# Optimization experiments

Measured on AMD Instinct MI355X. Metric: run time of the kernel, lower is better.

The kernel has to match this reference:

```python
import jax, jax.numpy as jnp
import numpy as np


def setup_inputs() -> dict:
    key = jax.random.key(0)
    k1, k2, k3 = jax.random.split(key, 3)
    B, C, H, W = 256, 1, 512, 512
    SIZE, OUT = 512, 1
    x = jax.random.normal(k1, (B, C, H, W), dtype=jnp.float32)
    weights = jax.random.normal(k2, (SIZE, 4 * C, OUT), dtype=jnp.float32)
    biases = jax.random.normal(k3, (SIZE, OUT), dtype=jnp.float32)
    return {"x": x, "weights": weights, "biases": biases}


def _corner_ring_means(x, size):
    """Mean of the L-shaped ring between the (i)x(i) and (i-1)x(i-1) corner
    squares, for all four corners, computed via a summed-area table.
    Returns [B, size, 4*C] with corner order (tl, tr, bl, br), matching the
    original torch cat along the channel axis."""
    B, C = x.shape[0], x.shape[1]
    idx = jnp.arange(size)

    def corner_square_sums(y):
        # summed-area table anchored at top-left of y
        S = jnp.cumsum(jnp.cumsum(y, axis=2), axis=3)
        # S[..., i-1, i-1] = sum of y[:, :, :i, :i]
        return S[:, :, idx, idx]  # [B, C, size]

    tl = corner_square_sums(x)
    tr = corner_square_sums(x[:, :, :, ::-1])
    bl = corner_square_sums(x[:, :, ::-1, :])
    br = corner_square_sums(x[:, :, ::-1, ::-1])
    sq = jnp.stack([tl, tr, bl, br], axis=-1)  # [B, C, size, 4]

    # ring sum_i = square_sum_i - square_sum_{i-1}
    prev = jnp.concatenate([jnp.zeros_like(sq[:, :, :1]), sq[:, :, :-1]], axis=2)
    # ring pixel count: i*i - (i-1)*(i-1) = 2i - 1
    denom = (2 * jnp.arange(1, size + 1) - 1).astype(x.dtype)
    means = (sq - prev) / denom[None, None, :, None]  # [B, C, size, 4]

    # match torch cat(dim=2) of four [B, size, C] tensors -> [B, size, 4*C]
    return jnp.transpose(means, (0, 2, 3, 1)).reshape(B, size, 4 * C)


def reference(x, weights, biases):
    size = weights.shape[0]
    feats = _corner_ring_means(x, size)               # [B, size, 4]
    # F.linear(x_i, weights[i].T, biases[i]) == x_i @ weights[i] + biases[i]
    out = jnp.einsum('bsf,sfo->bso', feats, weights) + biases[None]
    out = jax.nn.relu(out)                            # per-index activation
    # torch cat(dim=1) of [B, out] chunks then squeeze(-1); out=1 -> [B, size]
    return out.reshape(x.shape[0], -1)
```

## Files before the change

### kernel.cpp

```cpp
#include <hip/hip_runtime.h>


#define HH 512
#define WW 512
#define NRING 512
#define NB (4 * NRING)

template<bool PARTIALS>
__global__ __launch_bounds__(256)
void ring_sum_kernel(const float* __restrict__ x, float* __restrict__ ws) {
    __shared__ float bins[NB];
    __shared__ float sc[4][64][17];
    const int tid  = threadIdx.x;
    const int lane = tid & 63;
    const int wave = tid >> 6;
    const int b     = blockIdx.x >> 3;
    const int chunk = blockIdx.x & 7;

    for (int t = tid; t < NB; t += 256) bins[t] = 0.f;
    __syncthreads();

    float vTL[8] = {0,0,0,0,0,0,0,0};
    float vTR[8] = {0,0,0,0,0,0,0,0};
    float vBL[8] = {0,0,0,0,0,0,0,0};
    float vBR[8] = {0,0,0,0,0,0,0,0};
    float rTL[16], rTR[16], rBL[16], rBR[16];
    #pragma unroll
    for (int k = 0; k < 16; ++k) { rTL[k]=0.f; rTR[k]=0.f; rBL[k]=0.f; rBR[k]=0.f; }

    const float4* img = (const float4*)x + (size_t)b * (HH * WW / 4);
    const int cA = 4 * lane;
    const int cB = 256 + 4 * lane;
    const int rbase = chunk * 64 + wave * 16;
    const bool top = (rbase < 256);

    float4 bufA[3], bufB[3];
    {
        const float4* rp0 = img + (size_t)rbase * (WW / 4);
        bufA[0] = rp0[lane];  bufB[0] = rp0[64 + lane];
        const float4* rp1 = img + (size_t)(rbase + 1) * (WW / 4);
        bufA[1] = rp1[lane];  bufB[1] = rp1[64 + lane];
    }

    #pragma unroll
    for (int k = 0; k < 16; ++k) {
        const int cur = k % 3, nx = (k + 2) % 3;
        if (k < 14) {
            const float4* rp = img + (size_t)(rbase + k + 2) * (WW / 4);
            bufA[nx] = rp[lane];  bufB[nx] = rp[64 + lane];
        }
        const int r = rbase + k;
        const int s = 511 - r;
        const float4 a  = bufA[cur];
        const float4 bb = bufB[cur];

        if (top) {
            #pragma unroll
            for (int e = 0; e < 4; ++e) {
                float v = (&a.x)[e]; int c = cA + e;
                rBL[k] += v;
                vTR[e] += v;
                float sel  = (c <= r) ? v : 0.f; rTL[k] += sel;  vTL[e] += v - sel;
                float sel2 = (c >= r) ? v : 0.f; rBR[k] += sel2; vBR[e] += v - sel2;
            }
            #pragma unroll
            for (int e = 0; e < 4; ++e) {
                float v = (&bb.x)[e]; int c = cB + e;
                rBR[k] += v;
                vTL[4 + e] += v;
                float sel  = (c >= s) ? v : 0.f; rTR[k] += sel;  vTR[4 + e] += v - sel;
                float sel2 = (c <= s) ? v : 0.f; rBL[k] += sel2; vBL[4 + e] += v - sel2;
            }
        } else {
            #pragma unroll
            for (int e = 0; e < 4; ++e) {
                float v = (&a.x)[e]; int c = cA + e;
                rTL[k] += v;
                vBR[e] += v;
                float sel  = (c >= s) ? v : 0.f; rTR[k] += sel;  vTR[e] += v - sel;
                float sel2 = (c <= s) ? v : 0.f; rBL[k] += sel2; vBL[e] += v - sel2;
            }
            #pragma unroll
            for (int e = 0; e < 4; ++e) {
                float v = (&bb.x)[e]; int c = cB + e;
                rTR[k] += v;
                vBL[4 + e] += v;
                float sel  = (c <= r) ? v : 0.f; rTL[k] += sel;  vTL[4 + e] += v - sel;
                float sel2 = (c >= r) ? v : 0.f; rBR[k] += sel2; vBR[4 + e] += v - sel2;
            }
        }
    }

    const int q  = lane >> 4;
    const int kk = lane & 15;
#define REDUCE_CORNER(ARR, CIDX, RING_OF_KK)                                   \
    {                                                                          \
        _Pragma("unroll")                                                      \
        for (int j = 0; j < 16; ++j) sc[wave][lane][j] = ARR[j];               \
        __syncthreads();                                                       \
        float acc = 0.f;                                                       \
        _Pragma("unroll")                                                      \
        for (int l = 0; l < 16; ++l) acc += sc[wave][q * 16 + l][kk];          \
        acc += __shfl_down(acc, 32);                                           \
        acc += __shfl_down(acc, 16);                                           \
        if (lane < 16) atomicAdd(&bins[(CIDX) * NRING + (RING_OF_KK)], acc);   \
        __syncthreads();                                                       \
    }
    REDUCE_CORNER(rTL, 0, rbase + kk)
    REDUCE_CORNER(rTR, 1, rbase + kk)
    REDUCE_CORNER(rBL, 2, 511 - (rbase + kk))
    REDUCE_CORNER(rBR, 3, 511 - (rbase + kk))
#undef REDUCE_CORNER

    #pragma unroll
    for (int e = 0; e < 8; ++e) {
        int c = (e < 4) ? (cA + e) : (cB + e - 4);
        atomicAdd(&bins[0 * NRING + c],         vTL[e]);
        atomicAdd(&bins[1 * NRING + (511 - c)], vTR[e]);
        atomicAdd(&bins[2 * NRING + c],         vBL[e]);
        atomicAdd(&bins[3 * NRING + (511 - c)], vBR[e]);
    }
    __syncthreads();

    if (PARTIALS) {
        float* outp = ws + ((size_t)b * 8 + chunk) * NB;
        for (int t = tid; t < NB; t += 256) outp[t] = bins[t];
    } else {
        float* outp = ws + (size_t)b * NB;
        for (int t = tid; t < NB; t += 256) atomicAdd(&outp[t], bins[t]);
    }
}

__global__ __launch_bounds__(512)
void linear_kernel(const float* __restrict__ ws, const float* __restrict__ wts,
                   const float* __restrict__ bias, float* __restrict__ out,
                   int nparts) {
    const int b = blockIdx.x;
    const int i = threadIdx.x;
    const float* base = ws + (size_t)b * nparts * NB;
    float s0 = 0.f, s1 = 0.f, s2 = 0.f, s3 = 0.f;
    for (int p = 0; p < nparts; ++p) {
        const float* pb = base + (size_t)p * NB;
        s0 += pb[0 * NRING + i];
        s1 += pb[1 * NRING + i];
        s2 += pb[2 * NRING + i];
        s3 += pb[3 * NRING + i];
    }
    float4 w  = ((const float4*)wts)[i];
    float inv = 1.0f / (float)(2 * i + 1);
    float val = (s0 * w.x + s1 * w.y + s2 * w.z + s3 * w.w) * inv + bias[i];
    out[b * NRING + i] = fmaxf(val, 0.0f);
}

extern "C" void kernel_launch(void* const* d_in, const int* in_sizes, int n_in,
                              void* d_out, int out_size, void* d_ws, size_t ws_size,
                              hipStream_t stream) {
    const float* x    = (const float*)d_in[0];
    const float* wts  = (const float*)d_in[1];
    const float* bias = (const float*)d_in[2];
    float* out = (float*)d_out;

    const int B = in_sizes[0] / (HH * WW);
    float* ws = (float*)d_ws;

    const size_t need = (size_t)B * 8 * NB * sizeof(float);
    if (ws_size >= need) {
        ring_sum_kernel<true><<<dim3(B * 8), dim3(256), 0, stream>>>(x, ws);
        linear_kernel<<<dim3(B), dim3(512), 0, stream>>>(ws, wts, bias, out, 8);
    } else {
        hipMemsetAsync(ws, 0, (size_t)B * NB * sizeof(float), stream);
        ring_sum_kernel<false><<<dim3(B * 8), dim3(256), 0, stream>>>(x, ws);
        linear_kernel<<<dim3(B), dim3(512), 0, stream>>>(ws, wts, bias, out, 1);
    }
}
```

Baseline: 411.9 us.

## Stage image rows through LDS with async global_load_lds double buffering

Replaces the per-wave register triple-buffered row loads with block-wide direct global-to-LDS loads (global_load_lds) into a double-buffered 8-row tile, and interleaves rows across waves. The LDS tile shares storage with the epilogue scratch through a union. It also swizzles the chunk index per batch so concurrent blocks touch different row ranges. The goal is more memory-level parallelism and better coalescing for this bandwidth-bound pass, at the cost of a __syncthreads per tile and extra LDS traffic.

```diff
diff --git a/kernel.cpp b/kernel.cpp
--- a/kernel.cpp
+++ b/kernel.cpp
@@ -6,19 +6,19 @@
 #define NRING 512
 #define NB (4 * NRING)
 
+struct ShmMain { float tile[2][8][WW]; };
+struct ShmEpi  { float sc[4][64][17]; float bins[NB]; };
+
 template<bool PARTIALS>
 __global__ __launch_bounds__(256)
 void ring_sum_kernel(const float* __restrict__ x, float* __restrict__ ws) {
-    __shared__ float bins[NB];
-    __shared__ float sc[4][64][17];
+    __shared__ union { ShmMain m; ShmEpi e; } shm;
     const int tid  = threadIdx.x;
     const int lane = tid & 63;
     const int wave = tid >> 6;
-    const int b     = blockIdx.x >> 3;
-    const int chunk = blockIdx.x & 7;
-
-    for (int t = tid; t < NB; t += 256) bins[t] = 0.f;
-    __syncthreads();
+    const int idx   = blockIdx.x;
+    const int b     = idx >> 3;
+    const int chunk = (idx + (idx >> 3)) & 7;
 
     float vTL[8] = {0,0,0,0,0,0,0,0};
     float vTR[8] = {0,0,0,0,0,0,0,0};
@@ -28,106 +28,121 @@
     #pragma unroll
     for (int k = 0; k < 16; ++k) { rTL[k]=0.f; rTR[k]=0.f; rBL[k]=0.f; rBR[k]=0.f; }
 
-    const float4* img = (const float4*)x + (size_t)b * (HH * WW / 4);
+    const size_t imgF = (size_t)b * (HH * WW);
     const int cA = 4 * lane;
     const int cB = 256 + 4 * lane;
-    const int rbase = chunk * 64 + wave * 16;
-    const bool top = (rbase < 256);
+    const bool top = (chunk < 4);
 
-    float4 bufA[3], bufB[3];
-    {
-        const float4* rp0 = img + (size_t)rbase * (WW / 4);
-        bufA[0] = rp0[lane];  bufB[0] = rp0[64 + lane];
-        const float4* rp1 = img + (size_t)(rbase + 1) * (WW / 4);
-        bufA[1] = rp1[lane];  bufB[1] = rp1[64 + lane];
-    }
+#define STAGE(bufi, tt)                                                        \
+    do {                                                                       \
+        const float* gsrc = x + imgF + (size_t)(chunk * 64 + (tt) * 8) * WW    \
+                              + tid * 4;                                       \
+        float* ldst = &shm.m.tile[bufi][0][0] + tid * 4;                       \
+        _Pragma("unroll")                                                      \
+        for (int rr = 0; rr < 4; ++rr)                                         \
+            __builtin_amdgcn_global_load_lds(                                  \
+                (const __attribute__((address_space(1))) void*)(gsrc + rr * 1024), \
+                (__attribute__((address_space(3))) void*)(ldst + rr * 1024),   \
+                16, 0, 0);                                                     \
+    } while (0)
+
+    STAGE(0, 0);
+    __syncthreads();
 
     #pragma unroll
-    for (int k = 0; k < 16; ++k) {
-        const int cur = k % 3, nx = (k + 2) % 3;
-        if (k < 14) {
-            const float4* rp = img + (size_t)(rbase + k + 2) * (WW / 4);
-            bufA[nx] = rp[lane];  bufB[nx] = rp[64 + lane];
-        }
-        const int r = rbase + k;
-        const int s = 511 - r;
-        const float4 a  = bufA[cur];
-        const float4 bb = bufB[cur];
-
-        if (top) {
-            #pragma unroll
-            for (int e = 0; e < 4; ++e) {
-                float v = (&a.x)[e]; int c = cA + e;
-                rBL[k] += v;
-                vTR[e] += v;
-                float sel  = (c <= r) ? v : 0.f; rTL[k] += sel;  vTL[e] += v - sel;
-                float sel2 = (c >= r) ? v : 0.f; rBR[k] += sel2; vBR[e] += v - sel2;
-            }
-            #pragma unroll
-            for (int e = 0; e < 4; ++e) {
-                float v = (&bb.x)[e]; int c = cB + e;
-                rBR[k] += v;
-                vTL[4 + e] += v;
-                float sel  = (c >= s) ? v : 0.f; rTR[k] += sel;  vTR[4 + e] += v - sel;
-                float sel2 = (c <= s) ? v : 0.f; rBL[k] += sel2; vBL[4 + e] += v - sel2;
-            }
-        } else {
-            #pragma unroll
-            for (int e = 0; e < 4; ++e) {
-                float v = (&a.x)[e]; int c = cA + e;
-                rTL[k] += v;
-                vBR[e] += v;
-                float sel  = (c >= s) ? v : 0.f; rTR[k] += sel;  vTR[e] += v - sel;
-                float sel2 = (c <= s) ? v : 0.f; rBL[k] += sel2; vBL[e] += v - sel2;
-            }
-            #pragma unroll
-            for (int e = 0; e < 4; ++e) {
-                float v = (&bb.x)[e]; int c = cB + e;
-                rTR[k] += v;
-                vBL[4 + e] += v;
-                float sel  = (c <= r) ? v : 0.f; rTL[k] += sel;  vTL[4 + e] += v - sel;
-                float sel2 = (c >= r) ? v : 0.f; rBR[k] += sel2; vBR[4 + e] += v - sel2;
+    for (int t = 0; t < 8; ++t) {
+        if (t < 7) STAGE((t + 1) & 1, t + 1);
+        const int bufi = t & 1;
+        const int r0c = chunk * 64 + t * 8;
+        #pragma unroll
+        for (int jj = 0; jj < 2; ++jj) {
+            const int kloc = wave + 4 * jj;
+            const int r = r0c + kloc;
+            const int s = 511 - r;
+            const int j = 2 * t + jj;
+            const float4 a  = *(const float4*)&shm.m.tile[bufi][kloc][cA];
+            const float4 bb = *(const float4*)&shm.m.tile[bufi][kloc][cB];
+            if (top) {
+                #pragma unroll
+                for (int e = 0; e < 4; ++e) {
+                    float v = (&a.x)[e]; int c = cA + e;
+                    rBL[j] += v;
+                    vTR[e] += v;
+                    float sel  = (c <= r) ? v : 0.f; rTL[j] += sel;  vTL[e] += v - sel;
+                    float sel2 = (c >= r) ? v : 0.f; rBR[j] += sel2; vBR[e] += v - sel2;
+                }
+                #pragma unroll
+                for (int e = 0; e < 4; ++e) {
+                    float v = (&bb.x)[e]; int c = cB + e;
+                    rBR[j] += v;
+                    vTL[4 + e] += v;
+                    float sel  = (c >= s) ? v : 0.f; rTR[j] += sel;  vTR[4 + e] += v - sel;
+                    float sel2 = (c <= s) ? v : 0.f; rBL[j] += sel2; vBL[4 + e] += v - sel2;
+                }
+            } else {
+                #pragma unroll
+                for (int e = 0; e < 4; ++e) {
+                    float v = (&a.x)[e]; int c = cA + e;
+                    rTL[j] += v;
+                    vBR[e] += v;
+                    float sel  = (c >= s) ? v : 0.f; rTR[j] += sel;  vTR[e] += v - sel;
+                    float sel2 = (c <= s) ? v : 0.f; rBL[j] += sel2; vBL[e] += v - sel2;
+                }
+                #pragma unroll
+                for (int e = 0; e < 4; ++e) {
+                    float v = (&bb.x)[e]; int c = cB + e;
+                    rTR[j] += v;
+                    vBL[4 + e] += v;
+                    float sel  = (c <= r) ? v : 0.f; rTL[j] += sel;  vTL[4 + e] += v - sel;
+                    float sel2 = (c >= r) ? v : 0.f; rBR[j] += sel2; vBR[4 + e] += v - sel2;
+                }
             }
         }
+        __syncthreads();
     }
+#undef STAGE
+
+    for (int t2 = tid; t2 < NB; t2 += 256) shm.e.bins[t2] = 0.f;
+    __syncthreads();
 
     const int q  = lane >> 4;
     const int kk = lane & 15;
-#define REDUCE_CORNER(ARR, CIDX, RING_OF_KK)                                   \
+    const int rl = 8 * (kk >> 1) + wave + 4 * (kk & 1);
+#define REDUCE_CORNER(ARR, CIDX, RING)                                         \
     {                                                                          \
         _Pragma("unroll")                                                      \
-        for (int j = 0; j < 16; ++j) sc[wave][lane][j] = ARR[j];               \
+        for (int j2 = 0; j2 < 16; ++j2) shm.e.sc[wave][lane][j2] = ARR[j2];    \
         __syncthreads();                                                       \
         float acc = 0.f;                                                       \
         _Pragma("unroll")                                                      \
-        for (int l = 0; l < 16; ++l) acc += sc[wave][q * 16 + l][kk];          \
+        for (int l = 0; l < 16; ++l) acc += shm.e.sc[wave][q * 16 + l][kk];    \
         acc += __shfl_down(acc, 32);                                           \
         acc += __shfl_down(acc, 16);                                           \
-        if (lane < 16) atomicAdd(&bins[(CIDX) * NRING + (RING_OF_KK)], acc);   \
+        if (lane < 16) atomicAdd(&shm.e.bins[(CIDX) * NRING + (RING)], acc);   \
         __syncthreads();                                                       \
     }
-    REDUCE_CORNER(rTL, 0, rbase + kk)
-    REDUCE_CORNER(rTR, 1, rbase + kk)
-    REDUCE_CORNER(rBL, 2, 511 - (rbase + kk))
-    REDUCE_CORNER(rBR, 3, 511 - (rbase + kk))
+    REDUCE_CORNER(rTL, 0, chunk * 64 + rl)
+    REDUCE_CORNER(rTR, 1, chunk * 64 + rl)
+    REDUCE_CORNER(rBL, 2, 511 - (chunk * 64 + rl))
+    REDUCE_CORNER(rBR, 3, 511 - (chunk * 64 + rl))
 #undef REDUCE_CORNER
 
     #pragma unroll
     for (int e = 0; e < 8; ++e) {
         int c = (e < 4) ? (cA + e) : (cB + e - 4);
-        atomicAdd(&bins[0 * NRING + c],         vTL[e]);
-        atomicAdd(&bins[1 * NRING + (511 - c)], vTR[e]);
-        atomicAdd(&bins[2 * NRING + c],         vBL[e]);
-        atomicAdd(&bins[3 * NRING + (511 - c)], vBR[e]);
+        atomicAdd(&shm.e.bins[0 * NRING + c],         vTL[e]);
+        atomicAdd(&shm.e.bins[1 * NRING + (511 - c)], vTR[e]);
+        atomicAdd(&shm.e.bins[2 * NRING + c],         vBL[e]);
+        atomicAdd(&shm.e.bins[3 * NRING + (511 - c)], vBR[e]);
     }
     __syncthreads();
 
     if (PARTIALS) {
         float* outp = ws + ((size_t)b * 8 + chunk) * NB;
-        for (int t = tid; t < NB; t += 256) outp[t] = bins[t];
+        for (int t2 = tid; t2 < NB; t2 += 256) outp[t2] = shm.e.bins[t2];
     } else {
         float* outp = ws + (size_t)b * NB;
-        for (int t = tid; t < NB; t += 256) atomicAdd(&outp[t], bins[t]);
+        for (int t2 = tid; t2 < NB; t2 += 256) atomicAdd(&outp[t2], shm.e.bins[t2]);
     }
 }
 
```

Result: slower. 443.5 us (+7.7%).

## Split each image into 32 smaller row chunks and merge corner reductions

Applied to the files above, without the earlier changes.

Each block now processes 16 rows (4 per wave) instead of 64, quadrupling the grid and raising occupancy via launch bounds. All row loads are issued up front, and the four per-corner shared-memory reductions are merged into one pass with a single barrier. The linear kernel is split into 128-thread blocks and sums 32 partials. The cost is four times more partial-sum traffic and per-block bin initialization and atomics.

```diff
diff --git a/kernel.cpp b/kernel.cpp
--- a/kernel.cpp
+++ b/kernel.cpp
@@ -5,17 +5,19 @@
 #define WW 512
 #define NRING 512
 #define NB (4 * NRING)
+#define NCHUNK 32
+#define CROWS 16
 
 template<bool PARTIALS>
-__global__ __launch_bounds__(256)
+__global__ __launch_bounds__(256, 4)
 void ring_sum_kernel(const float* __restrict__ x, float* __restrict__ ws) {
     __shared__ float bins[NB];
     __shared__ float sc[4][64][17];
     const int tid  = threadIdx.x;
     const int lane = tid & 63;
     const int wave = tid >> 6;
-    const int b     = blockIdx.x >> 3;
-    const int chunk = blockIdx.x & 7;
+    const int b     = blockIdx.x >> 5;
+    const int chunk = blockIdx.x & 31;
 
     for (int t = tid; t < NB; t += 256) bins[t] = 0.f;
     __syncthreads();
@@ -24,36 +26,30 @@
     float vTR[8] = {0,0,0,0,0,0,0,0};
     float vBL[8] = {0,0,0,0,0,0,0,0};
     float vBR[8] = {0,0,0,0,0,0,0,0};
-    float rTL[16], rTR[16], rBL[16], rBR[16];
-    #pragma unroll
-    for (int k = 0; k < 16; ++k) { rTL[k]=0.f; rTR[k]=0.f; rBL[k]=0.f; rBR[k]=0.f; }
+    float rTL[4] = {0,0,0,0}, rTR[4] = {0,0,0,0};
+    float rBL[4] = {0,0,0,0}, rBR[4] = {0,0,0,0};
 
     const float4* img = (const float4*)x + (size_t)b * (HH * WW / 4);
     const int cA = 4 * lane;
     const int cB = 256 + 4 * lane;
-    const int rbase = chunk * 64 + wave * 16;
-    const bool top = (rbase < 256);
+    const int r0 = chunk * CROWS + wave * 4;
+    const bool top = (chunk < 16);
 
-    float4 bufA[3], bufB[3];
-    {
-        const float4* rp0 = img + (size_t)rbase * (WW / 4);
-        bufA[0] = rp0[lane];  bufB[0] = rp0[64 + lane];
-        const float4* rp1 = img + (size_t)(rbase + 1) * (WW / 4);
-        bufA[1] = rp1[lane];  bufB[1] = rp1[64 + lane];
+    float4 A[4], Bv[4];
+    #pragma unroll
+    for (int k = 0; k < 4; ++k) {
+        const float4* rp = img + (size_t)(r0 + k) * (WW / 4);
+        A[k]  = rp[lane];
+        Bv[k] = rp[64 + lane];
     }
+    __builtin_amdgcn_sched_barrier(0);
 
     #pragma unroll
-    for (int k = 0; k < 16; ++k) {
-        const int cur = k % 3, nx = (k + 2) % 3;
-        if (k < 14) {
-            const float4* rp = img + (size_t)(rbase + k + 2) * (WW / 4);
-            bufA[nx] = rp[lane];  bufB[nx] = rp[64 + lane];
-        }
-        const int r = rbase + k;
+    for (int k = 0; k < 4; ++k) {
+        const int r = r0 + k;
         const int s = 511 - r;
-        const float4 a  = bufA[cur];
-        const float4 bb = bufB[cur];
-
+        const float4 a  = A[k];
+        const float4 bb = Bv[k];
         if (top) {
             #pragma unroll
             for (int e = 0; e < 4; ++e) {
@@ -91,26 +87,29 @@
         }
     }
 
-    const int q  = lane >> 4;
-    const int kk = lane & 15;
-#define REDUCE_CORNER(ARR, CIDX, RING_OF_KK)                                   \
-    {                                                                          \
-        _Pragma("unroll")                                                      \
-        for (int j = 0; j < 16; ++j) sc[wave][lane][j] = ARR[j];               \
-        __syncthreads();                                                       \
-        float acc = 0.f;                                                       \
-        _Pragma("unroll")                                                      \
-        for (int l = 0; l < 16; ++l) acc += sc[wave][q * 16 + l][kk];          \
-        acc += __shfl_down(acc, 32);                                           \
-        acc += __shfl_down(acc, 16);                                           \
-        if (lane < 16) atomicAdd(&bins[(CIDX) * NRING + (RING_OF_KK)], acc);   \
-        __syncthreads();                                                       \
+    #pragma unroll
+    for (int k = 0; k < 4; ++k) {
+        sc[wave][lane][k * 4 + 0] = rTL[k];
+        sc[wave][lane][k * 4 + 1] = rTR[k];
+        sc[wave][lane][k * 4 + 2] = rBL[k];
+        sc[wave][lane][k * 4 + 3] = rBR[k];
     }
-    REDUCE_CORNER(rTL, 0, rbase + kk)
-    REDUCE_CORNER(rTR, 1, rbase + kk)
-    REDUCE_CORNER(rBL, 2, 511 - (rbase + kk))
-    REDUCE_CORNER(rBR, 3, 511 - (rbase + kk))
-#undef REDUCE_CORNER
+    __syncthreads();
+    {
+        const int q  = lane >> 4;
+        const int kk = lane & 15;
+        float acc = 0.f;
+        #pragma unroll
+        for (int l = 0; l < 16; ++l) acc += sc[wave][q * 16 + l][kk];
+        acc += __shfl_down(acc, 32);
+        acc += __shfl_down(acc, 16);
+        if (lane < 16) {
+            const int k = kk >> 2, corner = kk & 3;
+            const int r = r0 + k;
+            const int ring = (corner < 2) ? r : (511 - r);
+            atomicAdd(&bins[corner * NRING + ring], acc);
+        }
+    }
 
     #pragma unroll
     for (int e = 0; e < 8; ++e) {
@@ -123,7 +122,7 @@
     __syncthreads();
 
     if (PARTIALS) {
-        float* outp = ws + ((size_t)b * 8 + chunk) * NB;
+        float* outp = ws + ((size_t)b * NCHUNK + chunk) * NB;
         for (int t = tid; t < NB; t += 256) outp[t] = bins[t];
     } else {
         float* outp = ws + (size_t)b * NB;
@@ -131,12 +130,12 @@
     }
 }
 
-__global__ __launch_bounds__(512)
+__global__ __launch_bounds__(128)
 void linear_kernel(const float* __restrict__ ws, const float* __restrict__ wts,
                    const float* __restrict__ bias, float* __restrict__ out,
                    int nparts) {
-    const int b = blockIdx.x;
-    const int i = threadIdx.x;
+    const int b  = blockIdx.x >> 2;
+    const int i  = (blockIdx.x & 3) * 128 + threadIdx.x;
     const float* base = ws + (size_t)b * nparts * NB;
     float s0 = 0.f, s1 = 0.f, s2 = 0.f, s3 = 0.f;
     for (int p = 0; p < nparts; ++p) {
@@ -163,13 +162,13 @@
     const int B = in_sizes[0] / (HH * WW);
     float* ws = (float*)d_ws;
 
-    const size_t need = (size_t)B * 8 * NB * sizeof(float);
+    const size_t need = (size_t)B * NCHUNK * NB * sizeof(float);
     if (ws_size >= need) {
-        ring_sum_kernel<true><<<dim3(B * 8), dim3(256), 0, stream>>>(x, ws);
-        linear_kernel<<<dim3(B), dim3(512), 0, stream>>>(ws, wts, bias, out, 8);
+        ring_sum_kernel<true><<<dim3(B * NCHUNK), dim3(256), 0, stream>>>(x, ws);
+        linear_kernel<<<dim3(B * 4), dim3(128), 0, stream>>>(ws, wts, bias, out, NCHUNK);
     } else {
         hipMemsetAsync(ws, 0, (size_t)B * NB * sizeof(float), stream);
-        ring_sum_kernel<false><<<dim3(B * 8), dim3(256), 0, stream>>>(x, ws);
-        linear_kernel<<<dim3(B), dim3(512), 0, stream>>>(ws, wts, bias, out, 1);
+        ring_sum_kernel<false><<<dim3(B * NCHUNK), dim3(256), 0, stream>>>(x, ws);
+        linear_kernel<<<dim3(B * 4), dim3(128), 0, stream>>>(ws, wts, bias, out, 1);
     }
 }
```

Result: slower. 641.8 us (+55.8%).
